# Kernel optimization log

Measured on AMD Instinct MI355X. Metric: run time of the kernel, lower is better.

The kernel has to match this reference:

```python
import jax, jax.numpy as jnp
import numpy as np

N, D, E, C = 50000, 128, 500000, 2
K1, K2 = 3, 5


def spline_conv(x, src, dst, pseudo, W, root, bias, K, num_nodes):
    # degree-1 open B-spline basis over dim=1 pseudo coords in [0,1]
    v = pseudo[:, 0] * (K - 1)                      # [E]
    i0f = jnp.floor(v)
    frac = v - i0f                                   # [E]
    i0 = jnp.clip(i0f.astype(jnp.int32), 0, K - 1)
    i1 = jnp.clip(i0 + 1, 0, K - 1)
    xs = x[src]                                      # [E, D] gather
    # scatter basis-weighted neighbor feats into per-(node,kernel) buckets
    acc = jax.ops.segment_sum((1.0 - frac)[:, None] * xs, dst * K + i0,
                              num_segments=num_nodes * K)
    acc = acc + jax.ops.segment_sum(frac[:, None] * xs, dst * K + i1,
                                    num_segments=num_nodes * K)
    acc = acc.reshape(num_nodes, K, -1)              # [N, K, D]
    deg = jax.ops.segment_sum(jnp.ones_like(v), dst, num_segments=num_nodes)
    out = jnp.einsum('nkd,kdo->no', acc, W) / jnp.maximum(deg, 1.0)[:, None]
    return out + x @ root + bias                     # mean aggr + root + bias


def setup_inputs() -> dict:
    key = jax.random.key(0)
    ks = jax.random.split(key, 12)
    s = 1.0 / np.sqrt(D)
    return {
        'x': jax.random.normal(ks[0], (N, D), jnp.float32),
        'edge_index': jax.random.randint(ks[1], (2, E), 0, N, jnp.int64),
        'edge_attr': jax.random.uniform(ks[2], (E, 1), jnp.float32),
        'W1': jax.random.normal(ks[3], (K1, D, D), jnp.float32) * s,
        'root1': jax.random.normal(ks[4], (D, D), jnp.float32) * s,
        'b1': jnp.zeros((D,), jnp.float32),
        'W2': jax.random.normal(ks[5], (K2, D, D), jnp.float32) * s,
        'root2': jax.random.normal(ks[6], (D, D), jnp.float32) * s,
        'b2': jnp.zeros((D,), jnp.float32),
        'Wm': jax.random.normal(ks[7], (D, C), jnp.float32) * s,
        'bm': jnp.zeros((C,), jnp.float32),
    }


def reference(x, edge_index, edge_attr, W1, root1, b1, W2, root2, b2, Wm, bm):
    src, dst = edge_index[0], edge_index[1]
    h = jax.nn.elu(spline_conv(x, src, dst, edge_attr, W1, root1, b1, K1, N))
    # dropout is identity in eval mode
    h = jax.nn.elu(spline_conv(h, src, dst, edge_attr, W2, root2, b2, K2, N))
    return jax.nn.relu(h @ Wm + bm)                  # [N, C]
```

## Files before the change

kernel.cpp:

```cpp
#include <hip/hip_runtime.h>
#include <cmath>


typedef __attribute__((ext_vector_type(8))) short bf16x8;
typedef __attribute__((ext_vector_type(4))) float f32x4;

static inline int cdiv(int a, int b) { return (a + b - 1) / b; }

__device__ __forceinline__ float bf2f(unsigned short u) {
  unsigned v = ((unsigned)u) << 16;
  return __builtin_bit_cast(float, v);
}
__device__ __forceinline__ unsigned short f2bf(float f) {
  unsigned u = __builtin_bit_cast(unsigned, f);
  u += 0x7FFFu + ((u >> 16) & 1u);
  return (unsigned short)(u >> 16);
}
__device__ __forceinline__ float elu1(float v) {
  return v > 0.f ? v : (expf(v) - 1.f);
}

__global__ void hist_kernel(const int* __restrict__ ei, int E,
                            int* __restrict__ cnt) {
  int e = blockIdx.x * blockDim.x + threadIdx.x;
  if (e < E) atomicAdd(&cnt[ei[E + e]], 1);
}

__global__ void scan_partials_kernel(const int* __restrict__ cnt, int N,
                                     int* __restrict__ partials) {
  __shared__ int red[256];
  int base = blockIdx.x * 1024;
  int s = 0;
  for (int i = threadIdx.x; i < 1024; i += 256) {
    int idx = base + i;
    if (idx < N) s += cnt[idx];
  }
  red[threadIdx.x] = s;
  __syncthreads();
  for (int off = 128; off > 0; off >>= 1) {
    if (threadIdx.x < off) red[threadIdx.x] += red[threadIdx.x + off];
    __syncthreads();
  }
  if (threadIdx.x == 0) partials[blockIdx.x] = red[0];
}

__global__ void scan_pscan_kernel(const int* __restrict__ partials, int nb,
                                  int* __restrict__ pscan) {
  __shared__ int tmp[256];
  int t = threadIdx.x;
  int v = (t < nb) ? partials[t] : 0;
  tmp[t] = v;
  __syncthreads();
  for (int off = 1; off < 256; off <<= 1) {
    int u = (t >= off) ? tmp[t - off] : 0;
    __syncthreads();
    tmp[t] += u;
    __syncthreads();
  }
  pscan[t + 1] = tmp[t];
  if (t == 0) pscan[0] = 0;
}

__global__ void scan_apply_kernel(const int* __restrict__ cnt, int N,
                                  const int* __restrict__ pscan, int nb,
                                  int* __restrict__ rowptr, int* __restrict__ cursor) {
  __shared__ int tsum[256];
  int t = threadIdx.x;
  int base = blockIdx.x * 1024 + t * 4;
  int v0 = 0, v1 = 0, v2 = 0, v3 = 0;
  if (base + 0 < N) v0 = cnt[base + 0];
  if (base + 1 < N) v1 = cnt[base + 1];
  if (base + 2 < N) v2 = cnt[base + 2];
  if (base + 3 < N) v3 = cnt[base + 3];
  int s = v0 + v1 + v2 + v3;
  tsum[t] = s;
  __syncthreads();
  for (int off = 1; off < 256; off <<= 1) {
    int u = (t >= off) ? tsum[t - off] : 0;
    __syncthreads();
    tsum[t] += u;
    __syncthreads();
  }
  int excl = pscan[blockIdx.x] + tsum[t] - s;
  if (base + 0 < N) { rowptr[base + 0] = excl; cursor[base + 0] = excl; excl += v0; }
  if (base + 1 < N) { rowptr[base + 1] = excl; cursor[base + 1] = excl; excl += v1; }
  if (base + 2 < N) { rowptr[base + 2] = excl; cursor[base + 2] = excl; excl += v2; }
  if (base + 3 < N) { rowptr[base + 3] = excl; cursor[base + 3] = excl; excl += v3; }
  if (blockIdx.x == 0 && t == 0) rowptr[N] = pscan[nb];
}

__global__ void scatter_kernel(const int* __restrict__ ei,
                               const float* __restrict__ ea, int E,
                               int* __restrict__ cursor, int2* __restrict__ es) {
  int e = blockIdx.x * blockDim.x + threadIdx.x;
  if (e < E) {
    int dst = ei[E + e];
    int pos = atomicAdd(&cursor[dst], 1);
    es[pos] = make_int2(ei[e], __float_as_int(ea[e]));
  }
}

__global__ void cvt_x_kernel(const float* __restrict__ x,
                             unsigned short* __restrict__ xb, int n4) {
  for (int i = blockIdx.x * blockDim.x + threadIdx.x; i < n4;
       i += gridDim.x * blockDim.x) {
    float4 v = ((const float4*)x)[i];
    ushort4 o;
    o.x = f2bf(v.x); o.y = f2bf(v.y); o.z = f2bf(v.z); o.w = f2bf(v.w);
    ((ushort4*)xb)[i] = o;
  }
}

__global__ void build_btf_kernel(const float* __restrict__ W,
                                 const float* __restrict__ root,
                                 unsigned short* __restrict__ BtF, int KD, int KT) {
  int idx = blockIdx.x * blockDim.x + threadIdx.x;
  if (idx >= 128 * KT) return;
  int G = idx >> 9;
  int r = idx & 511;
  int lane = r >> 3;
  int j = r & 7;
  int ks = G >> 3;
  int ni = G & 7;
  int col = ni * 16 + (lane & 15);
  int k = ks * 32 + (lane >> 4) * 8 + j;
  float v = (k < KD) ? W[(size_t)k * 128 + col] : root[(size_t)(k - KD) * 128 + col];
  BtF[idx] = f2bf(v);
}

template <int K, int KT, bool FINAL>
__global__ __launch_bounds__(256, 4) void fused_layer(
    const unsigned short* __restrict__ Xc,
    const int* __restrict__ rowptr, const int2* __restrict__ es,
    const unsigned short* __restrict__ BtF,
    const float* __restrict__ bias,
    unsigned short* __restrict__ Hout,
    const float* __restrict__ Wm, const float* __restrict__ bm,
    float* __restrict__ FOut) {
  constexpr int LDK = KT + 8;
  constexpr int NKS = KT / 32;
  __shared__ unsigned short Asub[16][LDK];
  __shared__ float hred[4][16][2];

  const int w = threadIdx.x >> 6;
  const int lane = threadIdx.x & 63;
  const int lr = lane & 15;
  const int kg = lane >> 4;
  const int node0 = blockIdx.x * 16;

  const int g = lane >> 4;
  const int d16 = lane & 15;
  const int r = w * 4 + g;
  const int node = node0 + r;
  const int beg = rowptr[node];
  const int end = rowptr[node + 1];
  const int deg = end - beg;

  float acc[K][8];
#pragma unroll
  for (int k = 0; k < K; ++k)
#pragma unroll
    for (int j = 0; j < 8; ++j) acc[k][j] = 0.f;

  const int mx = max(max(__shfl(deg, 0), __shfl(deg, 16)),
                     max(__shfl(deg, 32), __shfl(deg, 48)));
  const int lastc = max(end - 1, 0);

  for (int s0 = 0; s0 < mx; s0 += 4) {
    int2 sp[4];
#pragma unroll
    for (int t = 0; t < 4; ++t) sp[t] = es[min(beg + s0 + t, lastc)];
    uint4 rv[4];
#pragma unroll
    for (int t = 0; t < 4; ++t)
      rv[t] = *(const uint4*)(Xc + (size_t)sp[t].x * 128 + d16 * 8);
#pragma unroll
    for (int t = 0; t < 4; ++t) {
      const bool ok = (s0 + t) < deg;
      const float v = ok ? __int_as_float(sp[t].y) * (float)(K - 1) : -2.f;
      float x[8];
      x[0] = __builtin_bit_cast(float, rv[t].x << 16);
      x[1] = __builtin_bit_cast(float, rv[t].x & 0xffff0000u);
      x[2] = __builtin_bit_cast(float, rv[t].y << 16);
      x[3] = __builtin_bit_cast(float, rv[t].y & 0xffff0000u);
      x[4] = __builtin_bit_cast(float, rv[t].z << 16);
      x[5] = __builtin_bit_cast(float, rv[t].z & 0xffff0000u);
      x[6] = __builtin_bit_cast(float, rv[t].w << 16);
      x[7] = __builtin_bit_cast(float, rv[t].w & 0xffff0000u);
#pragma unroll
      for (int k = 0; k < K; ++k) {
        const float wk = fmaxf(1.f - fabsf(v - (float)k), 0.f);
#pragma unroll
        for (int j = 0; j < 8; ++j) acc[k][j] = fmaf(wk, x[j], acc[k][j]);
      }
    }
  }

  const float sc = 1.f / fmaxf((float)deg, 1.f);
#pragma unroll
  for (int k = 0; k < K; ++k) {
    uint4 ov;
    ov.x = (unsigned)f2bf(acc[k][0] * sc) | ((unsigned)f2bf(acc[k][1] * sc) << 16);
    ov.y = (unsigned)f2bf(acc[k][2] * sc) | ((unsigned)f2bf(acc[k][3] * sc) << 16);
    ov.z = (unsigned)f2bf(acc[k][4] * sc) | ((unsigned)f2bf(acc[k][5] * sc) << 16);
    ov.w = (unsigned)f2bf(acc[k][6] * sc) | ((unsigned)f2bf(acc[k][7] * sc) << 16);
    *(uint4*)&Asub[r][k * 128 + d16 * 8] = ov;
  }
  uint4 ownv = *(const uint4*)(Xc + (size_t)node * 128 + d16 * 8);
  *(uint4*)&Asub[r][K * 128 + d16 * 8] = ownv;
  __syncthreads();

  const int ni0 = w * 2;
  f32x4 acc2[2];
  acc2[0] = {0.f, 0.f, 0.f, 0.f};
  acc2[1] = {0.f, 0.f, 0.f, 0.f};
#pragma unroll
  for (int ks = 0; ks < NKS; ++ks) {
    bf16x8 a = *(const bf16x8*)&Asub[lr][ks * 32 + kg * 8];
#pragma unroll
    for (int j = 0; j < 2; ++j) {
      bf16x8 b = *(const bf16x8*)(BtF + (size_t)(ks * 8 + ni0 + j) * 512 + lane * 8);
      acc2[j] = __builtin_amdgcn_mfma_f32_16x16x32_bf16(a, b, acc2[j], 0, 0, 0);
    }
  }

  float bv[2];
#pragma unroll
  for (int j = 0; j < 2; ++j) bv[j] = bias[(ni0 + j) * 16 + lr];

  if constexpr (!FINAL) {
#pragma unroll
    for (int rr = 0; rr < 4; ++rr) {
      int row = kg * 4 + rr;
      int onode = node0 + row;
#pragma unroll
      for (int j = 0; j < 2; ++j) {
        float h = elu1(acc2[j][rr] + bv[j]);
        Hout[(size_t)onode * 128 + (ni0 + j) * 16 + lr] = f2bf(h);
      }
    }
  } else {
    float wm0[2], wm1[2];
#pragma unroll
    for (int j = 0; j < 2; ++j) {
      float2 wv = *(const float2*)&Wm[((ni0 + j) * 16 + lr) * 2];
      wm0[j] = wv.x; wm1[j] = wv.y;
    }
#pragma unroll
    for (int rr = 0; rr < 4; ++rr) {
      int row = kg * 4 + rr;
      float t0 = 0.f, t1 = 0.f;
#pragma unroll
      for (int j = 0; j < 2; ++j) {
        float h = elu1(acc2[j][rr] + bv[j]);
        t0 = fmaf(h, wm0[j], t0);
        t1 = fmaf(h, wm1[j], t1);
      }
#pragma unroll
      for (int off = 8; off > 0; off >>= 1) {
        t0 += __shfl_down(t0, off);
        t1 += __shfl_down(t1, off);
      }
      if (lr == 0) {
        hred[w][row][0] = t0;
        hred[w][row][1] = t1;
      }
    }
    __syncthreads();
    if (threadIdx.x < 32) {
      int row = threadIdx.x >> 1;
      int c = threadIdx.x & 1;
      float s = hred[0][row][c] + hred[1][row][c] + hred[2][row][c] +
                hred[3][row][c] + bm[c];
      FOut[(size_t)(node0 + row) * 2 + c] = fmaxf(s, 0.f);
    }
  }
}

extern "C" void kernel_launch(void* const* d_in, const int* in_sizes, int n_in,
                              void* d_out, int out_size, void* d_ws, size_t ws_size,
                              hipStream_t stream) {
  const float* x = (const float*)d_in[0];
  const int* ei = (const int*)d_in[1];
  const float* ea = (const float*)d_in[2];
  const float* W1 = (const float*)d_in[3];
  const float* root1 = (const float*)d_in[4];
  const float* b1 = (const float*)d_in[5];
  const float* W2 = (const float*)d_in[6];
  const float* root2 = (const float*)d_in[7];
  const float* b2 = (const float*)d_in[8];
  const float* Wm = (const float*)d_in[9];
  const float* bm = (const float*)d_in[10];
  const int N = in_sizes[0] / 128;
  const int E = in_sizes[2];
  const int KT1 = 512, KT2 = 768;
  const int nb = cdiv(N, 1024);

  char* base = (char*)d_ws;
  size_t off = 0;
  auto alloc = [&](size_t bytes) -> void* {
    void* p = base + off;
    off += (bytes + 255) & ~(size_t)255;
    return p;
  };
  int* cnt = (int*)alloc((size_t)N * 4);
  int* rowptr = (int*)alloc((size_t)(N + 1) * 4);
  int* cursor = (int*)alloc((size_t)N * 4);
  int* partials = (int*)alloc(256 * 4);
  int* pscan = (int*)alloc(257 * 4);
  int2* es = (int2*)alloc((size_t)E * 8);
  unsigned short* xb = (unsigned short*)alloc((size_t)N * 128 * 2);
  unsigned short* h1 = (unsigned short*)alloc((size_t)N * 128 * 2);
  unsigned short* BtF1 = (unsigned short*)alloc((size_t)128 * KT1 * 2);
  unsigned short* BtF2 = (unsigned short*)alloc((size_t)128 * KT2 * 2);
  (void)ws_size; (void)n_in; (void)out_size;

  hipMemsetAsync(cnt, 0, (size_t)N * 4, stream);
  hist_kernel<<<cdiv(E, 256), 256, 0, stream>>>(ei, E, cnt);
  scan_partials_kernel<<<nb, 256, 0, stream>>>(cnt, N, partials);
  scan_pscan_kernel<<<1, 256, 0, stream>>>(partials, nb, pscan);
  scan_apply_kernel<<<nb, 256, 0, stream>>>(cnt, N, pscan, nb, rowptr, cursor);
  scatter_kernel<<<cdiv(E, 256), 256, 0, stream>>>(ei, ea, E, cursor, es);

  build_btf_kernel<<<cdiv(128 * KT1, 256), 256, 0, stream>>>(W1, root1, BtF1, 384, KT1);
  build_btf_kernel<<<cdiv(128 * KT2, 256), 256, 0, stream>>>(W2, root2, BtF2, 640, KT2);

  cvt_x_kernel<<<2048, 256, 0, stream>>>(x, xb, N * 32);

  const int nblk = N / 16;
  fused_layer<3, 512, false><<<nblk, 256, 0, stream>>>(
      xb, rowptr, es, BtF1, b1, h1, nullptr, nullptr, nullptr);
  fused_layer<5, 768, true><<<nblk, 256, 0, stream>>>(
      h1, rowptr, es, BtF2, b2, nullptr, Wm, bm, (float*)d_out);
}
```

Before: 163.9 us.

## Process 32 nodes per 512-thread block so each B fragment feeds two MFMAs

Each block now covers 32 nodes with 8 waves instead of 16 nodes with 4 waves. In the GEMM stage each wave owns one 16-column output tile and reuses each loaded weight fragment across two 16-row A tiles, which halves weight fragment loads per node. The final reduction sums over 8 waves, and bounds guards handle node counts that are not a multiple of 32. Shared memory per block doubles and the launch bounds change to 512 threads with 6 blocks, which may limit occupancy or registers.

```diff
diff --git a/kernel.cpp b/kernel.cpp
--- a/kernel.cpp
+++ b/kernel.cpp
@@ -129,29 +129,28 @@
 }
 
 template <int K, int KT, bool FINAL>
-__global__ __launch_bounds__(256, 4) void fused_layer(
+__global__ __launch_bounds__(512, 6) void fused_layer(
     const unsigned short* __restrict__ Xc,
     const int* __restrict__ rowptr, const int2* __restrict__ es,
     const unsigned short* __restrict__ BtF,
     const float* __restrict__ bias,
     unsigned short* __restrict__ Hout,
     const float* __restrict__ Wm, const float* __restrict__ bm,
-    float* __restrict__ FOut) {
+    float* __restrict__ FOut, int N) {
   constexpr int LDK = KT + 8;
   constexpr int NKS = KT / 32;
-  __shared__ unsigned short Asub[16][LDK];
-  __shared__ float hred[4][16][2];
+  __shared__ unsigned short Asub[32][LDK];
 
   const int w = threadIdx.x >> 6;
   const int lane = threadIdx.x & 63;
   const int lr = lane & 15;
   const int kg = lane >> 4;
-  const int node0 = blockIdx.x * 16;
+  const int node0 = blockIdx.x * 32;
 
   const int g = lane >> 4;
   const int d16 = lane & 15;
   const int r = w * 4 + g;
-  const int node = node0 + r;
+  const int node = min(node0 + r, N - 1);
   const int beg = rowptr[node];
   const int end = rowptr[node + 1];
   const int deg = end - beg;
@@ -210,69 +209,66 @@
   *(uint4*)&Asub[r][K * 128 + d16 * 8] = ownv;
   __syncthreads();
 
-  const int ni0 = w * 2;
-  f32x4 acc2[2];
-  acc2[0] = {0.f, 0.f, 0.f, 0.f};
-  acc2[1] = {0.f, 0.f, 0.f, 0.f};
+  const int ni = w;
+  f32x4 acc0 = {0.f, 0.f, 0.f, 0.f};
+  f32x4 acc1 = {0.f, 0.f, 0.f, 0.f};
 #pragma unroll
   for (int ks = 0; ks < NKS; ++ks) {
-    bf16x8 a = *(const bf16x8*)&Asub[lr][ks * 32 + kg * 8];
-#pragma unroll
-    for (int j = 0; j < 2; ++j) {
-      bf16x8 b = *(const bf16x8*)(BtF + (size_t)(ks * 8 + ni0 + j) * 512 + lane * 8);
-      acc2[j] = __builtin_amdgcn_mfma_f32_16x16x32_bf16(a, b, acc2[j], 0, 0, 0);
-    }
-  }
-
-  float bv[2];
-#pragma unroll
-  for (int j = 0; j < 2; ++j) bv[j] = bias[(ni0 + j) * 16 + lr];
+    bf16x8 b = *(const bf16x8*)(BtF + (size_t)(ks * 8 + ni) * 512 + lane * 8);
+    bf16x8 a0 = *(const bf16x8*)&Asub[lr][ks * 32 + kg * 8];
+    bf16x8 a1 = *(const bf16x8*)&Asub[16 + lr][ks * 32 + kg * 8];
+    acc0 = __builtin_amdgcn_mfma_f32_16x16x32_bf16(a0, b, acc0, 0, 0, 0);
+    acc1 = __builtin_amdgcn_mfma_f32_16x16x32_bf16(a1, b, acc1, 0, 0, 0);
+  }
+
+  const float bv = bias[ni * 16 + lr];
 
   if constexpr (!FINAL) {
 #pragma unroll
-    for (int rr = 0; rr < 4; ++rr) {
-      int row = kg * 4 + rr;
-      int onode = node0 + row;
-#pragma unroll
-      for (int j = 0; j < 2; ++j) {
-        float h = elu1(acc2[j][rr] + bv[j]);
-        Hout[(size_t)onode * 128 + (ni0 + j) * 16 + lr] = f2bf(h);
+    for (int mf = 0; mf < 2; ++mf) {
+      f32x4 a = mf ? acc1 : acc0;
+#pragma unroll
+      for (int rr = 0; rr < 4; ++rr) {
+        int onode = node0 + mf * 16 + kg * 4 + rr;
+        if (onode < N) {
+          float h = elu1(a[rr] + bv);
+          Hout[(size_t)onode * 128 + ni * 16 + lr] = f2bf(h);
+        }
       }
     }
   } else {
-    float wm0[2], wm1[2];
-#pragma unroll
-    for (int j = 0; j < 2; ++j) {
-      float2 wv = *(const float2*)&Wm[((ni0 + j) * 16 + lr) * 2];
-      wm0[j] = wv.x; wm1[j] = wv.y;
-    }
-#pragma unroll
-    for (int rr = 0; rr < 4; ++rr) {
-      int row = kg * 4 + rr;
-      float t0 = 0.f, t1 = 0.f;
-#pragma unroll
-      for (int j = 0; j < 2; ++j) {
-        float h = elu1(acc2[j][rr] + bv[j]);
-        t0 = fmaf(h, wm0[j], t0);
-        t1 = fmaf(h, wm1[j], t1);
-      }
-#pragma unroll
-      for (int off = 8; off > 0; off >>= 1) {
-        t0 += __shfl_down(t0, off);
-        t1 += __shfl_down(t1, off);
-      }
-      if (lr == 0) {
-        hred[w][row][0] = t0;
-        hred[w][row][1] = t1;
+    __shared__ float hred[8][32][2];
+    float2 wv = *(const float2*)&Wm[(ni * 16 + lr) * 2];
+#pragma unroll
+    for (int mf = 0; mf < 2; ++mf) {
+      f32x4 a = mf ? acc1 : acc0;
+#pragma unroll
+      for (int rr = 0; rr < 4; ++rr) {
+        float h = elu1(a[rr] + bv);
+        float t0 = h * wv.x;
+        float t1 = h * wv.y;
+#pragma unroll
+        for (int off = 8; off > 0; off >>= 1) {
+          t0 += __shfl_down(t0, off);
+          t1 += __shfl_down(t1, off);
+        }
+        if (lr == 0) {
+          hred[w][mf * 16 + kg * 4 + rr][0] = t0;
+          hred[w][mf * 16 + kg * 4 + rr][1] = t1;
+        }
       }
     }
     __syncthreads();
-    if (threadIdx.x < 32) {
+    if (threadIdx.x < 64) {
       int row = threadIdx.x >> 1;
       int c = threadIdx.x & 1;
-      float s = hred[0][row][c] + hred[1][row][c] + hred[2][row][c] +
-                hred[3][row][c] + bm[c];
-      FOut[(size_t)(node0 + row) * 2 + c] = fmaxf(s, 0.f);
+      int onode = node0 + row;
+      if (onode < N) {
+        float s = bm[c];
+#pragma unroll
+        for (int ww = 0; ww < 8; ++ww) s += hred[ww][row][c];
+        FOut[(size_t)onode * 2 + c] = fmaxf(s, 0.f);
+      }
     }
   }
 }
@@ -327,9 +323,9 @@
 
   cvt_x_kernel<<<2048, 256, 0, stream>>>(x, xb, N * 32);
 
-  const int nblk = N / 16;
-  fused_layer<3, 512, false><<<nblk, 256, 0, stream>>>(
-      xb, rowptr, es, BtF1, b1, h1, nullptr, nullptr, nullptr);
-  fused_layer<5, 768, true><<<nblk, 256, 0, stream>>>(
-      h1, rowptr, es, BtF2, b2, nullptr, Wm, bm, (float*)d_out);
-}
+  const int nblk = cdiv(N, 32);
+  fused_layer<3, 512, false><<<nblk, 512, 0, stream>>>(
+      xb, rowptr, es, BtF1, b1, h1, nullptr, nullptr, nullptr, N);
+  fused_layer<5, 768, true><<<nblk, 512, 0, stream>>>(
+      h1, rowptr, es, BtF2, b2, nullptr, Wm, bm, (float*)d_out, N);
+}
```

Result: slower. 232.6 us (+41.9%).

## Sort nodes by degree so each block's gather loop is balanced

Applied to the files above, without the earlier changes.

Adds a counting sort of nodes by in-degree (histogram, scan, scatter) and makes the fused layers process nodes in that permuted order, writing outputs through the permutation. Each wavefront's gather loop runs to the maximum degree of its four nodes, so grouping nodes of similar degree cuts wasted loop iterations on short rows. In exchange it adds three small kernels, an extra indirection, and scattered output writes and feature reads with less locality.

```diff
diff --git a/kernel.cpp b/kernel.cpp
--- a/kernel.cpp
+++ b/kernel.cpp
@@ -100,6 +100,34 @@
   }
 }
 
+__global__ void deg_hist_kernel(const int* __restrict__ rowptr, int N,
+                                int* __restrict__ bins) {
+  int i = blockIdx.x * blockDim.x + threadIdx.x;
+  if (i < N) {
+    int d = rowptr[i + 1] - rowptr[i];
+    atomicAdd(&bins[min(d, 63)], 1);
+  }
+}
+
+__global__ void deg_scan_kernel(const int* __restrict__ bins,
+                                int* __restrict__ binoff) {
+  if (threadIdx.x == 0 && blockIdx.x == 0) {
+    int s = 0;
+    for (int i = 0; i < 64; ++i) { binoff[i] = s; s += bins[i]; }
+  }
+}
+
+__global__ void deg_scatter_kernel(const int* __restrict__ rowptr, int N,
+                                   int* __restrict__ binoff,
+                                   int* __restrict__ perm) {
+  int i = blockIdx.x * blockDim.x + threadIdx.x;
+  if (i < N) {
+    int d = rowptr[i + 1] - rowptr[i];
+    int pos = atomicAdd(&binoff[min(d, 63)], 1);
+    perm[pos] = i;
+  }
+}
+
 __global__ void cvt_x_kernel(const float* __restrict__ x,
                              unsigned short* __restrict__ xb, int n4) {
   for (int i = blockIdx.x * blockDim.x + threadIdx.x; i < n4;
@@ -132,6 +160,7 @@
 __global__ __launch_bounds__(256, 4) void fused_layer(
     const unsigned short* __restrict__ Xc,
     const int* __restrict__ rowptr, const int2* __restrict__ es,
+    const int* __restrict__ perm,
     const unsigned short* __restrict__ BtF,
     const float* __restrict__ bias,
     unsigned short* __restrict__ Hout,
@@ -151,7 +180,7 @@
   const int g = lane >> 4;
   const int d16 = lane & 15;
   const int r = w * 4 + g;
-  const int node = node0 + r;
+  const int node = perm[node0 + r];
   const int beg = rowptr[node];
   const int end = rowptr[node + 1];
   const int deg = end - beg;
@@ -232,7 +261,7 @@
 #pragma unroll
     for (int rr = 0; rr < 4; ++rr) {
       int row = kg * 4 + rr;
-      int onode = node0 + row;
+      int onode = perm[node0 + row];
 #pragma unroll
       for (int j = 0; j < 2; ++j) {
         float h = elu1(acc2[j][rr] + bv[j]);
@@ -270,9 +299,10 @@
     if (threadIdx.x < 32) {
       int row = threadIdx.x >> 1;
       int c = threadIdx.x & 1;
+      int onode = perm[node0 + row];
       float s = hred[0][row][c] + hred[1][row][c] + hred[2][row][c] +
                 hred[3][row][c] + bm[c];
-      FOut[(size_t)(node0 + row) * 2 + c] = fmaxf(s, 0.f);
+      FOut[(size_t)onode * 2 + c] = fmaxf(s, 0.f);
     }
   }
 }
@@ -308,6 +338,9 @@
   int* cursor = (int*)alloc((size_t)N * 4);
   int* partials = (int*)alloc(256 * 4);
   int* pscan = (int*)alloc(257 * 4);
+  int* bins = (int*)alloc(64 * 4);
+  int* binoff = (int*)alloc(64 * 4);
+  int* perm = (int*)alloc((size_t)N * 4);
   int2* es = (int2*)alloc((size_t)E * 8);
   unsigned short* xb = (unsigned short*)alloc((size_t)N * 128 * 2);
   unsigned short* h1 = (unsigned short*)alloc((size_t)N * 128 * 2);
@@ -316,12 +349,17 @@
   (void)ws_size; (void)n_in; (void)out_size;
 
   hipMemsetAsync(cnt, 0, (size_t)N * 4, stream);
+  hipMemsetAsync(bins, 0, 64 * 4, stream);
   hist_kernel<<<cdiv(E, 256), 256, 0, stream>>>(ei, E, cnt);
   scan_partials_kernel<<<nb, 256, 0, stream>>>(cnt, N, partials);
   scan_pscan_kernel<<<1, 256, 0, stream>>>(partials, nb, pscan);
   scan_apply_kernel<<<nb, 256, 0, stream>>>(cnt, N, pscan, nb, rowptr, cursor);
   scatter_kernel<<<cdiv(E, 256), 256, 0, stream>>>(ei, ea, E, cursor, es);
 
+  deg_hist_kernel<<<cdiv(N, 256), 256, 0, stream>>>(rowptr, N, bins);
+  deg_scan_kernel<<<1, 64, 0, stream>>>(bins, binoff);
+  deg_scatter_kernel<<<cdiv(N, 256), 256, 0, stream>>>(rowptr, N, binoff, perm);
+
   build_btf_kernel<<<cdiv(128 * KT1, 256), 256, 0, stream>>>(W1, root1, BtF1, 384, KT1);
   build_btf_kernel<<<cdiv(128 * KT2, 256), 256, 0, stream>>>(W2, root2, BtF2, 640, KT2);
 
@@ -329,7 +367,7 @@
 
   const int nblk = N / 16;
   fused_layer<3, 512, false><<<nblk, 256, 0, stream>>>(
-      xb, rowptr, es, BtF1, b1, h1, nullptr, nullptr, nullptr);
+      xb, rowptr, es, perm, BtF1, b1, h1, nullptr, nullptr, nullptr);
   fused_layer<5, 768, true><<<nblk, 256, 0, stream>>>(
-      h1, rowptr, es, BtF2, b2, nullptr, Wm, bm, (float*)d_out);
-}
+      h1, rowptr, es, perm, BtF2, b2, nullptr, Wm, bm, (float*)d_out);
+}
```

New measurement: 495.3 us. +202.1%, slower.
